# Kernel optimization log

Measured on AMD Instinct MI355X. Metric: run time of the kernel, lower is better.

Reference implementation:

```python
import jax, jax.numpy as jnp
import numpy as np
from jax import lax

S, D_IN, D_FC, H_LSTM, H_RNN, D_OUT = 16384, 6, 20, 48, 24, 2


def _lstm_layer(seq, Wih, Whh, bih, bhh):
    # seq: [S, d_in]; PyTorch gate order: i, f, g, o
    H = Whh.shape[1]
    xW = seq @ Wih.T + (bih + bhh)  # [S, 4H] precomputed input projections

    def step(carry, xw):
        h, c = carry
        g = xw + h @ Whh.T
        i = jax.nn.sigmoid(g[:H])
        f = jax.nn.sigmoid(g[H:2 * H])
        gg = jnp.tanh(g[2 * H:3 * H])
        o = jax.nn.sigmoid(g[3 * H:])
        c = f * c + i * gg
        h = o * jnp.tanh(c)
        return (h, c), h

    z = jnp.zeros((H,), seq.dtype)
    _, hs = lax.scan(step, (z, z), xW)
    return hs  # [S, H]


def _rnn_layer(seq, Wih, Whh, bih, bhh):
    H = Whh.shape[1]
    xW = seq @ Wih.T + (bih + bhh)

    def step(h, xw):
        h = jnp.tanh(xw + h @ Whh.T)
        return h, h

    _, hs = lax.scan(step, jnp.zeros((H,), seq.dtype), xW)
    return hs


def setup_inputs() -> dict:
    key = jax.random.key(0)
    ks = iter(jax.random.split(key, 32))

    def p(shape, fan_in):
        s = 1.0 / np.sqrt(fan_in)
        return jax.random.uniform(next(ks), shape, jnp.float32, -s, s)

    inp = {"x": jax.random.normal(next(ks), (S, D_IN), jnp.float32)}
    inp["fc1_W"] = p((D_FC, D_IN), D_IN)
    inp["fc1_b"] = p((D_FC,), D_IN)
    inp["fc2_W"] = p((D_FC, D_FC), D_FC)
    inp["fc2_b"] = p((D_FC,), D_FC)
    # LSTM layer 0: input 20 -> hidden 48
    inp["lstm0_Wih"] = p((4 * H_LSTM, D_FC), H_LSTM)
    inp["lstm0_Whh"] = p((4 * H_LSTM, H_LSTM), H_LSTM)
    inp["lstm0_bih"] = p((4 * H_LSTM,), H_LSTM)
    inp["lstm0_bhh"] = p((4 * H_LSTM,), H_LSTM)
    # LSTM layers 1..4: input 48 -> hidden 48, stacked
    inp["lstmr_Wih"] = p((4, 4 * H_LSTM, H_LSTM), H_LSTM)
    inp["lstmr_Whh"] = p((4, 4 * H_LSTM, H_LSTM), H_LSTM)
    inp["lstmr_bih"] = p((4, 4 * H_LSTM), H_LSTM)
    inp["lstmr_bhh"] = p((4, 4 * H_LSTM), H_LSTM)
    # RNN layer 0: 48 -> 24, layer 1: 24 -> 24
    inp["rnn0_Wih"] = p((H_RNN, H_LSTM), H_RNN)
    inp["rnn0_Whh"] = p((H_RNN, H_RNN), H_RNN)
    inp["rnn0_bih"] = p((H_RNN,), H_RNN)
    inp["rnn0_bhh"] = p((H_RNN,), H_RNN)
    inp["rnn1_Wih"] = p((H_RNN, H_RNN), H_RNN)
    inp["rnn1_Whh"] = p((H_RNN, H_RNN), H_RNN)
    inp["rnn1_bih"] = p((H_RNN,), H_RNN)
    inp["rnn1_bhh"] = p((H_RNN,), H_RNN)
    inp["fc4_W"] = p((D_OUT, H_RNN), H_RNN)
    inp["fc4_b"] = p((D_OUT,), H_RNN)
    return inp


def reference(x, fc1_W, fc1_b, fc2_W, fc2_b,
              lstm0_Wih, lstm0_Whh, lstm0_bih, lstm0_bhh,
              lstmr_Wih, lstmr_Whh, lstmr_bih, lstmr_bhh,
              rnn0_Wih, rnn0_Whh, rnn0_bih, rnn0_bhh,
              rnn1_Wih, rnn1_Whh, rnn1_bih, rnn1_bhh,
              fc4_W, fc4_b):
    h = jax.nn.relu(x @ fc1_W.T + fc1_b)
    h = jax.nn.relu(h @ fc2_W.T + fc2_b)
    h = _lstm_layer(h, lstm0_Wih, lstm0_Whh, lstm0_bih, lstm0_bhh)
    for l in range(4):  # fixed small layer loop
        h = _lstm_layer(h, lstmr_Wih[l], lstmr_Whh[l], lstmr_bih[l], lstmr_bhh[l])
    h = _rnn_layer(h, rnn0_Wih, rnn0_Whh, rnn0_bih, rnn0_bhh)
    h = _rnn_layer(h, rnn1_Wih, rnn1_Whh, rnn1_bih, rnn1_bhh)
    h = jax.nn.relu(h)
    out = h @ fc4_W.T + fc4_b  # [S, 2]
    return out[None]  # [1, S, 2] matching batch_first torch output
```

## Files before the change

### kernel.cpp

```cpp
#include <hip/hip_runtime.h>
#include <hip/hip_bf16.h>

#define S_LEN 16384
#define N_IN 23
#define CH2 32
#define NCH2 (S_LEN / CH2)
#define RING_D 8

#define XW_PAR_F4 1632
#define XW_FLOATS (2 * XW_PAR_F4 * 4)
#define L2E   1.442695041f
#define TWO_L2E 2.885390082f

typedef float v2f __attribute__((ext_vector_type(2)));
typedef _Float16 h2v __attribute__((ext_vector_type(2)));

__device__ __forceinline__ float fexp2(float x) {
#if __has_builtin(__builtin_amdgcn_exp2f)
    return __builtin_amdgcn_exp2f(x);
#else
    return exp2f(x);
#endif
}
__device__ __forceinline__ float fsig(float x) {
    return __builtin_amdgcn_rcpf(1.f + __expf(-x));
}
__device__ __forceinline__ float ftanh_fast(float x) {
    float e = __expf(-2.f * fabsf(x));
    float r = (1.f - e) * __builtin_amdgcn_rcpf(1.f + e);
    return x >= 0.f ? r : -r;
}
__device__ __forceinline__ float rlane(float v, int k) {
    return __uint_as_float(__builtin_amdgcn_readlane(__float_as_uint(v), k));
}
__device__ __forceinline__ h2v rlane_h2(h2v v, int k) {
    int b;
    __builtin_memcpy(&b, &v, 4);
    b = __builtin_amdgcn_readlane(b, k);
    h2v r;
    __builtin_memcpy(&r, &b, 4);
    return r;
}
__device__ __forceinline__ h2v pack_h2(float a, float b) {
    auto p = __builtin_amdgcn_cvt_pkrtz(a, b);
    h2v r;
    __builtin_memcpy(&r, &p, 4);
    return r;
}
__device__ __forceinline__ float dpp_xor1(float v) {
    int b = __float_as_int(v);
    int r = __builtin_amdgcn_update_dpp(b, b, 0xB1, 0xF, 0xF, false);
    return __int_as_float(r);
}

#if __has_builtin(__builtin_amdgcn_fdot2)
__device__ __forceinline__ float fdot2_hw(h2v w, h2v h, float acc) {
    return __builtin_amdgcn_fdot2(w, h, acc, false);
}
#define FDOT2(w, h, acc) fdot2_hw((w), (h), (acc))
#else
__device__ __forceinline__ float fdot2_sw(h2v w, h2v h, float acc) {
    return acc + (float)w.x * (float)h.x + (float)w.y * (float)h.y;
}
#define FDOT2(w, h, acc) fdot2_sw((w), (h), (acc))
#endif

__global__ void detect_kernel(const void* probe, int nsamp, int* flag)
{
    if (blockIdx.x == 0 && threadIdx.x == 0) {
        const unsigned short* p = (const unsigned short*)probe;
        int isbf16 = 1;
        for (int i = 0; i < nsamp; i++) {
            float v = __uint_as_float(((unsigned int)p[i]) << 16);
            if (!(fabsf(v) < 1e4f)) { isbf16 = 0; break; }
        }
        *flag = isbf16;
    }
}

struct IngestArgs {
    const void* src[N_IN];
    float*      dst[N_IN];
    int         n[N_IN];
};

__global__ void ingest_kernel(IngestArgs args, const int* __restrict__ flag)
{
    const int isbf16 = *flag;
    const int tid    = blockIdx.x * blockDim.x + threadIdx.x;
    const int stride = gridDim.x * blockDim.x;
    for (int i = 0; i < N_IN; i++) {
        const int n = args.n[i];
        float* dst  = args.dst[i];
        if (isbf16) {
            const unsigned short* s = (const unsigned short*)args.src[i];
            for (int j = tid; j < n; j += stride)
                dst[j] = __uint_as_float(((unsigned int)s[j]) << 16);
        } else {
            const float* s = (const float*)args.src[i];
            for (int j = tid; j < n; j += stride)
                dst[j] = s[j];
        }
    }
}

__global__ void init_kernel(int* prog)
{
    int t = threadIdx.x;
    if (t < 1024) prog[t] = 0;
}

__global__ void fc12_kernel(const float* __restrict__ x,
                            const float* __restrict__ W1, const float* __restrict__ b1,
                            const float* __restrict__ W2, const float* __restrict__ b2,
                            float* __restrict__ h2out)
{
    int s = blockIdx.x * blockDim.x + threadIdx.x;
    if (s >= S_LEN) return;
    float xin[6];
#pragma unroll
    for (int k = 0; k < 6; k++) xin[k] = x[s * 6 + k];
    float h1[20];
#pragma unroll
    for (int j = 0; j < 20; j++) {
        float a = b1[j];
#pragma unroll
        for (int k = 0; k < 6; k++) a += W1[j * 6 + k] * xin[k];
        h1[j] = a > 0.f ? a : 0.f;
    }
#pragma unroll
    for (int j = 0; j < 20; j++) {
        float a = b2[j];
#pragma unroll
        for (int k = 0; k < 20; k++) a += W2[j * 20 + k] * h1[k];
        h2out[s * 20 + j] = a > 0.f ? a : 0.f;
    }
}

template <int DIN, int NG, bool TRANS>
__device__ void producer_block(const float* __restrict__ in,
                               const float* __restrict__ Wih,
                               const float* __restrict__ bih,
                               const float* __restrict__ bhh,
                               float* __restrict__ ring,
                               int* my_prog, int* in_prog, int* cons_prog,
                               float* smem)
{
    constexpr int GR  = NG / 3;
    constexpr int GS  = 256 / GR;
    constexpr int SLT = CH2 / GS;

    const int t  = threadIdx.x;
    const int rg = t % GR;
    const int sg = t / GR;

    float* in_sh = smem;
    float* xw_sh = smem + CH2 * DIN;

    float w[3][DIN];
    float bs[3];
    int cellr[3], partr[3];
#pragma unroll
    for (int r = 0; r < 3; r++) {
        const int row = rg * 3 + r;
        const float fac = TRANS ? ((row / 48) == 2 ? TWO_L2E : L2E) : 1.f;
#pragma unroll
        for (int k = 0; k < DIN; k++) w[r][k] = Wih[row * DIN + k] * fac;
        bs[r] = (bih[row] + bhh[row]) * fac;
        cellr[r] = row % 48;
        partr[r] = row / 48;
    }

    const float4* x4 = (const float4*)in_sh;

    for (int c = 0; c < NCH2; c++) {
        if (t == 0) {
            if (in_prog) {
                while (__hip_atomic_load(in_prog, __ATOMIC_ACQUIRE, __HIP_MEMORY_SCOPE_AGENT) < c + 1)
                    __builtin_amdgcn_s_sleep(1);
            }
            if (c >= RING_D) {
                while (__hip_atomic_load(cons_prog, __ATOMIC_ACQUIRE, __HIP_MEMORY_SCOPE_AGENT) < c - RING_D + 1)
                    __builtin_amdgcn_s_sleep(1);
            }
        }
        __syncthreads();
        {
            const float4* gsrc = (const float4*)(in + (size_t)c * CH2 * DIN);
            float4* ldst = (float4*)in_sh;
            for (int i = t; i < CH2 * DIN / 4; i += 256) ldst[i] = gsrc[i];
        }
        __syncthreads();

#pragma unroll
        for (int i = 0; i < SLT; i++) {
            const int sl = sg * SLT + i;
            float a0 = bs[0], a1 = bs[1], a2 = bs[2];
#pragma unroll
            for (int k = 0; k < DIN / 4; k++) {
                float4 xv = x4[sl * (DIN / 4) + k];
                a0 += w[0][4 * k + 0] * xv.x; a0 += w[0][4 * k + 1] * xv.y;
                a0 += w[0][4 * k + 2] * xv.z; a0 += w[0][4 * k + 3] * xv.w;
                a1 += w[1][4 * k + 0] * xv.x; a1 += w[1][4 * k + 1] * xv.y;
                a1 += w[1][4 * k + 2] * xv.z; a1 += w[1][4 * k + 3] * xv.w;
                a2 += w[2][4 * k + 0] * xv.x; a2 += w[2][4 * k + 1] * xv.y;
                a2 += w[2][4 * k + 2] * xv.z; a2 += w[2][4 * k + 3] * xv.w;
            }
            if (TRANS) {
                xw_sh[(sl * 48 + cellr[0]) * 4 + partr[0]] = a0;
                xw_sh[(sl * 48 + cellr[1]) * 4 + partr[1]] = a1;
                xw_sh[(sl * 48 + cellr[2]) * 4 + partr[2]] = a2;
            } else {
                xw_sh[sl * NG + rg * 3 + 0] = a0;
                xw_sh[sl * NG + rg * 3 + 1] = a1;
                xw_sh[sl * NG + rg * 3 + 2] = a2;
            }
        }
        __syncthreads();
        {
            const float4* lsrc = (const float4*)xw_sh;
            float4* gdst = (float4*)(ring + (size_t)(c % RING_D) * CH2 * NG);
            for (int i = t; i < CH2 * NG / 4; i += 256) gdst[i] = lsrc[i];
        }
        __syncthreads();
        if (t == 0)
            __hip_atomic_store(my_prog, c + 1, __ATOMIC_RELEASE, __HIP_MEMORY_SCOPE_AGENT);
    }
}

__device__ void lstm_scan(const float* __restrict__ Whh,
                          const float* __restrict__ ring,
                          float* __restrict__ hseq,
                          int* my_prog, int* prod_prog, float* smem)
{
    const int t = threadIdx.x;
    const int j = (t < 48) ? t : 47;
    float* xw_buf = smem;
    float* hh_buf = smem + XW_FLOATS;

    h2v wI[24], wF[24], wG[24], wO[24];
    if (t < 64) {
#pragma unroll
        for (int k = 0; k < 24; k++) {
            wI[k] = pack_h2(Whh[j * 48 + 2 * k] * L2E,           Whh[j * 48 + 2 * k + 1] * L2E);
            wF[k] = pack_h2(Whh[(48 + j) * 48 + 2 * k] * L2E,    Whh[(48 + j) * 48 + 2 * k + 1] * L2E);
            wG[k] = pack_h2(Whh[(96 + j) * 48 + 2 * k] * TWO_L2E, Whh[(96 + j) * 48 + 2 * k + 1] * TWO_L2E);
            wO[k] = pack_h2(Whh[(144 + j) * 48 + 2 * k] * L2E,   Whh[(144 + j) * 48 + 2 * k + 1] * L2E);
        }
    }
    const int jo = j + (j >> 4);
    float hvec = 0.f, ccell = 0.f;

    if (t >= 128) {
        while (__hip_atomic_load(prod_prog, __ATOMIC_ACQUIRE, __HIP_MEMORY_SCOPE_AGENT) < 1)
            __builtin_amdgcn_s_sleep(8);
        const float4* g = (const float4*)ring;
        float4* d = (float4*)xw_buf;
        for (int i = t - 128; i < CH2 * 48; i += 128) d[i + (i >> 4)] = g[i];
    }
    __syncthreads();

    for (int c = 0; c < NCH2; c++) {
        if (t < 64) {
            const float4* xf = (const float4*)xw_buf + (c & 1) * XW_PAR_F4;
            float* hh = hh_buf + (c & 1) * (CH2 * 48);
            float4 xw4 = xf[jo];
            for (int sl = 0; sl < CH2; sl++) {
                float4 nxt = xf[(sl + 1) * 51 + jo];
                float hn = dpp_xor1(hvec);
                h2v hp = pack_h2(hvec, hn);
                float aI0 = xw4.x, aF0 = xw4.y, aG0 = xw4.z, aO0 = xw4.w;
                float aI1 = 0.f, aF1 = 0.f, aG1 = 0.f, aO1 = 0.f;
#pragma unroll
                for (int kp = 0; kp < 12; kp++) {
                    h2v hb = rlane_h2(hp, 2 * kp);
                    aI0 = FDOT2(wI[kp], hb, aI0);
                    aF0 = FDOT2(wF[kp], hb, aF0);
                    aG0 = FDOT2(wG[kp], hb, aG0);
                    aO0 = FDOT2(wO[kp], hb, aO0);
                }
#pragma unroll
                for (int kp = 12; kp < 24; kp++) {
                    h2v hb = rlane_h2(hp, 2 * kp);
                    aI1 = FDOT2(wI[kp], hb, aI1);
                    aF1 = FDOT2(wF[kp], hb, aF1);
                    aG1 = FDOT2(wG[kp], hb, aG1);
                    aO1 = FDOT2(wO[kp], hb, aO1);
                }
                float aI = aI0 + aI1, aF = aF0 + aF1;
                float aG = aG0 + aG1, aO = aO0 + aO1;
                float eI = fexp2(-aI);
                float eF = fexp2(-aF);
                float eG = fexp2(-fabsf(aG));
                float eO = fexp2(-aO);
                float fv = __builtin_amdgcn_rcpf(1.f + eF);
                float ig = (1.f - eG) * __builtin_amdgcn_rcpf((1.f + eI) * (1.f + eG));
                ig = __int_as_float(__float_as_int(ig) ^
                                    (__float_as_int(aG) & 0x80000000));
                ccell = fmaf(fv, ccell, ig);
                float eC = fexp2(-TWO_L2E * fabsf(ccell));
                float r  = (1.f - eC) * __builtin_amdgcn_rcpf((1.f + eO) * (1.f + eC));
                float h  = __int_as_float(__float_as_int(r) ^
                                          (__float_as_int(ccell) & 0x80000000));
                hvec = h;
                if (t < 48) hh[sl * 48 + t] = h;
                xw4 = nxt;
            }
        } else if (t < 128) {
            if (c >= 1) {
                const float4* s4 = (const float4*)(hh_buf + ((c - 1) & 1) * (CH2 * 48));
                float4* d4 = (float4*)(hseq + (size_t)(c - 1) * CH2 * 48);
                for (int i = t - 64; i < CH2 * 12; i += 64) d4[i] = s4[i];
                if (t == 64)
                    __hip_atomic_store(my_prog, c, __ATOMIC_RELEASE, __HIP_MEMORY_SCOPE_AGENT);
            }
        } else {
            if (c + 1 < NCH2) {
                while (__hip_atomic_load(prod_prog, __ATOMIC_ACQUIRE, __HIP_MEMORY_SCOPE_AGENT) < c + 2)
                    __builtin_amdgcn_s_sleep(8);
                const float4* g = (const float4*)(ring + (size_t)((c + 1) % RING_D) * CH2 * 192);
                float4* d = (float4*)xw_buf + ((c + 1) & 1) * XW_PAR_F4;
                for (int i = t - 128; i < CH2 * 48; i += 128) d[i + (i >> 4)] = g[i];
            }
        }
        __syncthreads();
    }
    if (t >= 64 && t < 128) {
        const float4* s4 = (const float4*)(hh_buf + ((NCH2 - 1) & 1) * (CH2 * 48));
        float4* d4 = (float4*)(hseq + (size_t)(NCH2 - 1) * CH2 * 48);
        for (int i = t - 64; i < CH2 * 12; i += 64) d4[i] = s4[i];
        if (t == 64)
            __hip_atomic_store(my_prog, NCH2, __ATOMIC_RELEASE, __HIP_MEMORY_SCOPE_AGENT);
    }
}

__device__ void rnn_scan(const float* __restrict__ Whh,
                         const float* __restrict__ ring,
                         float* __restrict__ hseq,
                         int* my_prog, int* prod_prog, float* smem)
{
    const int t = threadIdx.x;
    float* xw_buf = smem;
    float* hh_buf = smem + 1536;

    float whh[24];
    if (t < 24) {
#pragma unroll
        for (int k = 0; k < 24; k++) whh[k] = Whh[t * 24 + k];
    }
    float hvec = 0.f;

    if (t >= 128) {
        while (__hip_atomic_load(prod_prog, __ATOMIC_ACQUIRE, __HIP_MEMORY_SCOPE_AGENT) < 1)
            __builtin_amdgcn_s_sleep(8);
        const float4* g = (const float4*)ring;
        float4* d = (float4*)xw_buf;
        for (int i = t - 128; i < CH2 * 6; i += 128) d[i] = g[i];
    }
    __syncthreads();

    for (int c = 0; c < NCH2; c++) {
        if (t < 64) {
            const float* xwc = xw_buf + (c & 1) * (CH2 * 24);
            float* hh = hh_buf + (c & 1) * (CH2 * 24);
            float xwv = (t < 24) ? xwc[t] : 0.f;
            for (int sl = 0; sl < CH2; sl++) {
                float nxtx = (t < 24) ? xwc[((sl + 1 < CH2) ? sl + 1 : sl) * 24 + t] : 0.f;
                float a0 = xwv, a1 = 0.f, a2 = 0.f, a3 = 0.f;
#pragma unroll
                for (int k = 0; k < 24; k += 4) {
                    a0 += rlane(hvec, k + 0) * whh[k + 0];
                    a1 += rlane(hvec, k + 1) * whh[k + 1];
                    a2 += rlane(hvec, k + 2) * whh[k + 2];
                    a3 += rlane(hvec, k + 3) * whh[k + 3];
                }
                float h = ftanh_fast((a0 + a1) + (a2 + a3));
                if (t < 24) {
                    hvec = h;
                    hh[sl * 24 + t] = h;
                }
                xwv = nxtx;
            }
        } else if (t < 128) {
            if (c >= 1) {
                const float4* s4 = (const float4*)(hh_buf + ((c - 1) & 1) * (CH2 * 24));
                float4* d4 = (float4*)(hseq + (size_t)(c - 1) * CH2 * 24);
                for (int i = t - 64; i < CH2 * 6; i += 64) d4[i] = s4[i];
                if (t == 64)
                    __hip_atomic_store(my_prog, c, __ATOMIC_RELEASE, __HIP_MEMORY_SCOPE_AGENT);
            }
        } else {
            if (c + 1 < NCH2) {
                while (__hip_atomic_load(prod_prog, __ATOMIC_ACQUIRE, __HIP_MEMORY_SCOPE_AGENT) < c + 2)
                    __builtin_amdgcn_s_sleep(8);
                const float4* g = (const float4*)(ring + (size_t)((c + 1) % RING_D) * CH2 * 24);
                float4* d = (float4*)(xw_buf + ((c + 1) & 1) * (CH2 * 24));
                for (int i = t - 128; i < CH2 * 6; i += 128) d[i] = g[i];
            }
        }
        __syncthreads();
    }
    if (t >= 64 && t < 128) {
        const float4* s4 = (const float4*)(hh_buf + ((NCH2 - 1) & 1) * (CH2 * 24));
        float4* d4 = (float4*)(hseq + (size_t)(NCH2 - 1) * CH2 * 24);
        for (int i = t - 64; i < CH2 * 6; i += 64) d4[i] = s4[i];
        if (t == 64)
            __hip_atomic_store(my_prog, NCH2, __ATOMIC_RELEASE, __HIP_MEMORY_SCOPE_AGENT);
    }
}

struct PipeArgs {
    const float* h2;
    const float* l0_Wih; const float* l0_Whh; const float* l0_bih; const float* l0_bhh;
    const float* lr_Wih; const float* lr_Whh; const float* lr_bih; const float* lr_bhh;
    const float* r0_Wih; const float* r0_Whh; const float* r0_bih; const float* r0_bhh;
    const float* r1_Wih; const float* r1_Whh; const float* r1_bih; const float* r1_bhh;
    float* seq0; float* seq1; float* seq2; float* seq3; float* seq4;
    float* rnnA; float* rnnB;
    float* ring[7];
    int* prog;
};

__global__ void __launch_bounds__(256, 1) pipeline_kernel(PipeArgs a)
{
    __shared__ __align__(16) float smem[16128];
    const int b = blockIdx.x;
    const float* seqin[7] = {a.h2, a.seq0, a.seq1, a.seq2, a.seq3, a.seq4, a.rnnA};
    float* seqout[7] = {a.seq0, a.seq1, a.seq2, a.seq3, a.seq4, a.rnnA, a.rnnB};
    int* sp[7]; int* pp[7];
    for (int l = 0; l < 7; l++) { sp[l] = a.prog + l * 64; pp[l] = a.prog + (8 + l) * 64; }

    if (b < 7) {
        const int l = b;
        int* inp = (l == 0) ? nullptr : sp[l - 1];
        if (l == 0) {
            producer_block<20, 192, true>(a.h2, a.l0_Wih, a.l0_bih, a.l0_bhh,
                                          a.ring[0], pp[0], inp, sp[0], smem);
        } else if (l <= 4) {
            producer_block<48, 192, true>(seqin[l],
                                          a.lr_Wih + (size_t)(l - 1) * 192 * 48,
                                          a.lr_bih + (size_t)(l - 1) * 192,
                                          a.lr_bhh + (size_t)(l - 1) * 192,
                                          a.ring[l], pp[l], inp, sp[l], smem);
        } else if (l == 5) {
            producer_block<48, 24, false>(a.seq4, a.r0_Wih, a.r0_bih, a.r0_bhh,
                                          a.ring[5], pp[5], inp, sp[5], smem);
        } else {
            producer_block<24, 24, false>(a.rnnA, a.r1_Wih, a.r1_bih, a.r1_bhh,
                                          a.ring[6], pp[6], inp, sp[6], smem);
        }
    } else {
        const int l = b - 7;
        if (l == 0) {
            lstm_scan(a.l0_Whh, a.ring[0], seqout[0], sp[0], pp[0], smem);
        } else if (l <= 4) {
            lstm_scan(a.lr_Whh + (size_t)(l - 1) * 192 * 48,
                      a.ring[l], seqout[l], sp[l], pp[l], smem);
        } else if (l == 5) {
            rnn_scan(a.r0_Whh, a.ring[5], seqout[5], sp[5], pp[5], smem);
        } else {
            rnn_scan(a.r1_Whh, a.ring[6], seqout[6], sp[6], pp[6], smem);
        }
    }
}

__global__ void out_kernel(const float* __restrict__ hin,
                           const float* __restrict__ W,
                           const float* __restrict__ b,
                           void* __restrict__ out,
                           const int* __restrict__ flag)
{
    int s = blockIdx.x * blockDim.x + threadIdx.x;
    if (s >= S_LEN) return;
    const int isbf16 = *flag;
    float h[24];
#pragma unroll
    for (int k = 0; k < 24; k++) {
        float v = hin[s * 24 + k];
        h[k] = v > 0.f ? v : 0.f;
    }
#pragma unroll
    for (int j = 0; j < 2; j++) {
        float a = b[j];
#pragma unroll
        for (int k = 0; k < 24; k++) a += W[j * 24 + k] * h[k];
        if (isbf16) ((__hip_bfloat16*)out)[s * 2 + j] = __float2bfloat16(a);
        else        ((float*)out)[s * 2 + j] = a;
    }
}

extern "C" void kernel_launch(void* const* d_in, const int* in_sizes, int n_in,
                              void* d_out, int out_size, void* d_ws, size_t ws_size,
                              hipStream_t stream)
{
    int*   ip    = (int*)d_ws;
    int*   flag  = ip;
    int*   prog  = ip + 256;
    float* ws    = (float*)d_ws;
    float* conv0 = ws + 4096;

    IngestArgs ia;
    float* conv[N_IN];
    {
        float* p = conv0;
        for (int i = 0; i < N_IN; i++) {
            conv[i] = p;
            ia.src[i] = d_in[i];
            ia.dst[i] = p;
            ia.n[i]   = in_sizes[i];
            p += in_sizes[i];
        }
    }
    float* h2   = conv0 + 191000;
    float* seq0 = h2 + 327680;
    float* seq1 = seq0 + 786432;
    float* seq2 = seq1 + 786432;
    float* seq3 = seq2 + 786432;
    float* seq4 = seq3 + 786432;
    float* rnnA = seq4 + 786432;
    float* rnnB = rnnA + 393216;
    float* rbase = rnnB + 393216;
    float* ring[7];
    {
        float* p = rbase;
        for (int l = 0; l < 5; l++) { ring[l] = p; p += RING_D * CH2 * 192; }
        for (int l = 5; l < 7; l++) { ring[l] = p; p += RING_D * CH2 * 24;  }
    }

    const int TPB = 256;
    const int NB  = S_LEN / TPB;

    detect_kernel<<<1, 64, 0, stream>>>(d_in[1], in_sizes[1], flag);
    ingest_kernel<<<128, 256, 0, stream>>>(ia, flag);
    init_kernel<<<1, 1024, 0, stream>>>(prog);

    fc12_kernel<<<NB, TPB, 0, stream>>>(conv[0], conv[1], conv[2], conv[3], conv[4], h2);

    PipeArgs pa;
    pa.h2 = h2;
    pa.l0_Wih = conv[5];  pa.l0_Whh = conv[6];  pa.l0_bih = conv[7];  pa.l0_bhh = conv[8];
    pa.lr_Wih = conv[9];  pa.lr_Whh = conv[10]; pa.lr_bih = conv[11]; pa.lr_bhh = conv[12];
    pa.r0_Wih = conv[13]; pa.r0_Whh = conv[14]; pa.r0_bih = conv[15]; pa.r0_bhh = conv[16];
    pa.r1_Wih = conv[17]; pa.r1_Whh = conv[18]; pa.r1_bih = conv[19]; pa.r1_bhh = conv[20];
    pa.seq0 = seq0; pa.seq1 = seq1; pa.seq2 = seq2; pa.seq3 = seq3; pa.seq4 = seq4;
    pa.rnnA = rnnA; pa.rnnB = rnnB;
    for (int l = 0; l < 7; l++) pa.ring[l] = ring[l];
    pa.prog = prog;

    pipeline_kernel<<<14, 256, 0, stream>>>(pa);

    out_kernel<<<NB, TPB, 0, stream>>>(rnnB, conv[21], conv[22], d_out, flag);
}
```

Measured before the change: 5.536 ms.

## Interleave two recurrent layers per wavefront with a chunk lag to hide latency

Each scan block now runs two consecutive recurrent layers (LSTM+LSTM or LSTM+RNN), offset by a fixed chunk lag. Their independent step chains are interleaved in one wavefront so the dependency latency of one layer's recurrence can be filled with the other's work. Chunk size is halved to shorten the pipeline fill, the padded shared-memory layout is dropped, and the launch goes from 14 to 11 blocks. The cost is double the weight registers per thread and more synchronisation points per chunk, and the halved chunk alters the ring buffer depth, which may cost throughput.

Result: slower. 9.692 ms (+75.1%).

```diff
diff --git a/kernel.cpp b/kernel.cpp
--- a/kernel.cpp
+++ b/kernel.cpp
@@ -3,16 +3,14 @@
 
 #define S_LEN 16384
 #define N_IN 23
-#define CH2 32
+#define CH2 16
 #define NCH2 (S_LEN / CH2)
 #define RING_D 8
-
-#define XW_PAR_F4 1632
-#define XW_FLOATS (2 * XW_PAR_F4 * 4)
-#define L2E   1.442695041f
+#define LAG 6
+
+#define L2E     1.442695041f
 #define TWO_L2E 2.885390082f
 
-typedef float v2f __attribute__((ext_vector_type(2)));
 typedef _Float16 h2v __attribute__((ext_vector_type(2)));
 
 __device__ __forceinline__ float fexp2(float x) {
@@ -21,9 +19,6 @@
 #else
     return exp2f(x);
 #endif
-}
-__device__ __forceinline__ float fsig(float x) {
-    return __builtin_amdgcn_rcpf(1.f + __expf(-x));
 }
 __device__ __forceinline__ float ftanh_fast(float x) {
     float e = __expf(-2.f * fabsf(x));
@@ -148,7 +143,7 @@
 {
     constexpr int GR  = NG / 3;
     constexpr int GS  = 256 / GR;
-    constexpr int SLT = CH2 / GS;
+    constexpr int SLT = (CH2 + GS - 1) / GS;
 
     const int t  = threadIdx.x;
     const int rg = t % GR;
@@ -195,25 +190,27 @@
 #pragma unroll
         for (int i = 0; i < SLT; i++) {
             const int sl = sg * SLT + i;
-            float a0 = bs[0], a1 = bs[1], a2 = bs[2];
-#pragma unroll
-            for (int k = 0; k < DIN / 4; k++) {
-                float4 xv = x4[sl * (DIN / 4) + k];
-                a0 += w[0][4 * k + 0] * xv.x; a0 += w[0][4 * k + 1] * xv.y;
-                a0 += w[0][4 * k + 2] * xv.z; a0 += w[0][4 * k + 3] * xv.w;
-                a1 += w[1][4 * k + 0] * xv.x; a1 += w[1][4 * k + 1] * xv.y;
-                a1 += w[1][4 * k + 2] * xv.z; a1 += w[1][4 * k + 3] * xv.w;
-                a2 += w[2][4 * k + 0] * xv.x; a2 += w[2][4 * k + 1] * xv.y;
-                a2 += w[2][4 * k + 2] * xv.z; a2 += w[2][4 * k + 3] * xv.w;
-            }
-            if (TRANS) {
-                xw_sh[(sl * 48 + cellr[0]) * 4 + partr[0]] = a0;
-                xw_sh[(sl * 48 + cellr[1]) * 4 + partr[1]] = a1;
-                xw_sh[(sl * 48 + cellr[2]) * 4 + partr[2]] = a2;
-            } else {
-                xw_sh[sl * NG + rg * 3 + 0] = a0;
-                xw_sh[sl * NG + rg * 3 + 1] = a1;
-                xw_sh[sl * NG + rg * 3 + 2] = a2;
+            if (sl < CH2) {
+                float a0 = bs[0], a1 = bs[1], a2 = bs[2];
+#pragma unroll
+                for (int k = 0; k < DIN / 4; k++) {
+                    float4 xv = x4[sl * (DIN / 4) + k];
+                    a0 += w[0][4 * k + 0] * xv.x; a0 += w[0][4 * k + 1] * xv.y;
+                    a0 += w[0][4 * k + 2] * xv.z; a0 += w[0][4 * k + 3] * xv.w;
+                    a1 += w[1][4 * k + 0] * xv.x; a1 += w[1][4 * k + 1] * xv.y;
+                    a1 += w[1][4 * k + 2] * xv.z; a1 += w[1][4 * k + 3] * xv.w;
+                    a2 += w[2][4 * k + 0] * xv.x; a2 += w[2][4 * k + 1] * xv.y;
+                    a2 += w[2][4 * k + 2] * xv.z; a2 += w[2][4 * k + 3] * xv.w;
+                }
+                if (TRANS) {
+                    xw_sh[(sl * 48 + cellr[0]) * 4 + partr[0]] = a0;
+                    xw_sh[(sl * 48 + cellr[1]) * 4 + partr[1]] = a1;
+                    xw_sh[(sl * 48 + cellr[2]) * 4 + partr[2]] = a2;
+                } else {
+                    xw_sh[sl * NG + rg * 3 + 0] = a0;
+                    xw_sh[sl * NG + rg * 3 + 1] = a1;
+                    xw_sh[sl * NG + rg * 3 + 2] = a2;
+                }
             }
         }
         __syncthreads();
@@ -228,109 +225,271 @@
     }
 }
 
-__device__ void lstm_scan(const float* __restrict__ Whh,
-                          const float* __restrict__ ring,
-                          float* __restrict__ hseq,
-                          int* my_prog, int* prod_prog, float* smem)
+__device__ __forceinline__ void lstm_step(
+    const h2v (&wI)[24], const h2v (&wF)[24], const h2v (&wG)[24], const h2v (&wO)[24],
+    const float4* __restrict__ xfl,
+    int sl, float4& xw4, float& hvec, float& ccell,
+    float*& hst, int hstr)
+{
+    float4 nxt = xfl[(sl + 1) * 48];
+    float hn = dpp_xor1(hvec);
+    h2v hp = pack_h2(hvec, hn);
+    float aI = xw4.x, aF = xw4.y, aG = xw4.z, aO = xw4.w;
+#pragma unroll
+    for (int kp = 0; kp < 24; kp++) {
+        h2v hb = rlane_h2(hp, 2 * kp);
+        aI = FDOT2(wI[kp], hb, aI);
+        aF = FDOT2(wF[kp], hb, aF);
+        aG = FDOT2(wG[kp], hb, aG);
+        aO = FDOT2(wO[kp], hb, aO);
+    }
+    float eI = fexp2(-aI);
+    float eF = fexp2(-aF);
+    float eG = fexp2(-fabsf(aG));
+    float eO = fexp2(-aO);
+    float fv = __builtin_amdgcn_rcpf(1.f + eF);
+    float ig = (1.f - eG) * __builtin_amdgcn_rcpf((1.f + eI) * (1.f + eG));
+    ig = __int_as_float(__float_as_int(ig) ^ (__float_as_int(aG) & 0x80000000));
+    ccell = fmaf(fv, ccell, ig);
+    float eC = fexp2(-TWO_L2E * fabsf(ccell));
+    float r  = (1.f - eC) * __builtin_amdgcn_rcpf((1.f + eO) * (1.f + eC));
+    float h  = __int_as_float(__float_as_int(r) ^ (__float_as_int(ccell) & 0x80000000));
+    hvec = h;
+    *hst = h; hst += hstr;
+    xw4 = nxt;
+}
+
+__device__ __forceinline__ void lstm_load_w(const float* __restrict__ Whh, int j,
+    h2v (&wI)[24], h2v (&wF)[24], h2v (&wG)[24], h2v (&wO)[24])
+{
+#pragma unroll
+    for (int k = 0; k < 24; k++) {
+        wI[k] = pack_h2(Whh[j * 48 + 2 * k] * L2E,            Whh[j * 48 + 2 * k + 1] * L2E);
+        wF[k] = pack_h2(Whh[(48 + j) * 48 + 2 * k] * L2E,     Whh[(48 + j) * 48 + 2 * k + 1] * L2E);
+        wG[k] = pack_h2(Whh[(96 + j) * 48 + 2 * k] * TWO_L2E, Whh[(96 + j) * 48 + 2 * k + 1] * TWO_L2E);
+        wO[k] = pack_h2(Whh[(144 + j) * 48 + 2 * k] * L2E,    Whh[(144 + j) * 48 + 2 * k + 1] * L2E);
+    }
+}
+
+__device__ __forceinline__ void rnn_step(
+    const float (&whh)[24], const float* __restrict__ xwc,
+    int sl, float& xwv, float& hvec, float*& hst, int hstr, int tB)
+{
+    float nxtx = xwc[(sl + 1) * 24 + tB];
+    float a0 = xwv, a1 = 0.f, a2 = 0.f, a3 = 0.f;
+#pragma unroll
+    for (int k = 0; k < 24; k += 4) {
+        a0 += rlane(hvec, k + 0) * whh[k + 0];
+        a1 += rlane(hvec, k + 1) * whh[k + 1];
+        a2 += rlane(hvec, k + 2) * whh[k + 2];
+        a3 += rlane(hvec, k + 3) * whh[k + 3];
+    }
+    float h = ftanh_fast((a0 + a1) + (a2 + a3));
+    hvec = h;
+    *hst = h; hst += hstr;
+    xwv = nxtx;
+}
+
+__device__ void lstm_scan_pair(
+    const float* __restrict__ WhhA, const float* __restrict__ ringA,
+    float* __restrict__ hseqA, int* spA, int* ppA,
+    const float* __restrict__ WhhB, const float* __restrict__ ringB,
+    float* __restrict__ hseqB, int* spB, int* ppB,
+    float* __restrict__ smem)
 {
     const int t = threadIdx.x;
     const int j = (t < 48) ? t : 47;
-    float* xw_buf = smem;
-    float* hh_buf = smem + XW_FLOATS;
-
-    h2v wI[24], wF[24], wG[24], wO[24];
+    float* xwA  = smem;
+    float* xwB  = smem + 6144;
+    float* hhA  = smem + 12288;
+    float* hhB  = smem + 13824;
+    float* dump = smem + 15360;
+
+    h2v wIA[24], wFA[24], wGA[24], wOA[24];
+    h2v wIB[24], wFB[24], wGB[24], wOB[24];
     if (t < 64) {
-#pragma unroll
-        for (int k = 0; k < 24; k++) {
-            wI[k] = pack_h2(Whh[j * 48 + 2 * k] * L2E,           Whh[j * 48 + 2 * k + 1] * L2E);
-            wF[k] = pack_h2(Whh[(48 + j) * 48 + 2 * k] * L2E,    Whh[(48 + j) * 48 + 2 * k + 1] * L2E);
-            wG[k] = pack_h2(Whh[(96 + j) * 48 + 2 * k] * TWO_L2E, Whh[(96 + j) * 48 + 2 * k + 1] * TWO_L2E);
-            wO[k] = pack_h2(Whh[(144 + j) * 48 + 2 * k] * L2E,   Whh[(144 + j) * 48 + 2 * k + 1] * L2E);
-        }
-    }
-    const int jo = j + (j >> 4);
-    float hvec = 0.f, ccell = 0.f;
+        lstm_load_w(WhhA, j, wIA, wFA, wGA, wOA);
+        lstm_load_w(WhhB, j, wIB, wFB, wGB, wOB);
+    }
+    float hA = 0.f, cAc = 0.f, hB = 0.f, cBc = 0.f;
+    const int hstr = (t < 48) ? 48 : 0;
 
     if (t >= 128) {
-        while (__hip_atomic_load(prod_prog, __ATOMIC_ACQUIRE, __HIP_MEMORY_SCOPE_AGENT) < 1)
+        while (__hip_atomic_load(ppA, __ATOMIC_ACQUIRE, __HIP_MEMORY_SCOPE_AGENT) < 1)
             __builtin_amdgcn_s_sleep(8);
-        const float4* g = (const float4*)ring;
-        float4* d = (float4*)xw_buf;
-        for (int i = t - 128; i < CH2 * 48; i += 128) d[i + (i >> 4)] = g[i];
+        const float4* g = (const float4*)ringA;
+        float4* d = (float4*)xwA;
+        for (int i = t - 128; i < CH2 * 48; i += 128) d[i] = g[i];
     }
     __syncthreads();
 
-    for (int c = 0; c < NCH2; c++) {
+    for (int cc = 0; cc < NCH2 + LAG; cc++) {
+        const int ca = cc, cb = cc - LAG;
+        const bool Aact = ca < NCH2;
+        const bool Bact = cb >= 0;
         if (t < 64) {
-            const float4* xf = (const float4*)xw_buf + (c & 1) * XW_PAR_F4;
-            float* hh = hh_buf + (c & 1) * (CH2 * 48);
-            float4 xw4 = xf[jo];
-            for (int sl = 0; sl < CH2; sl++) {
-                float4 nxt = xf[(sl + 1) * 51 + jo];
-                float hn = dpp_xor1(hvec);
-                h2v hp = pack_h2(hvec, hn);
-                float aI0 = xw4.x, aF0 = xw4.y, aG0 = xw4.z, aO0 = xw4.w;
-                float aI1 = 0.f, aF1 = 0.f, aG1 = 0.f, aO1 = 0.f;
-#pragma unroll
-                for (int kp = 0; kp < 12; kp++) {
-                    h2v hb = rlane_h2(hp, 2 * kp);
-                    aI0 = FDOT2(wI[kp], hb, aI0);
-                    aF0 = FDOT2(wF[kp], hb, aF0);
-                    aG0 = FDOT2(wG[kp], hb, aG0);
-                    aO0 = FDOT2(wO[kp], hb, aO0);
+            const float4* xfA = (const float4*)(xwA + (ca & 1) * (CH2 * 192)) + j;
+            const float4* xfB = (const float4*)(xwB + (cb & 1) * (CH2 * 192)) + j;
+            float* hsA = (t < 48) ? (hhA + (ca & 1) * (CH2 * 48) + t) : (dump + (t - 48));
+            float* hsB = (t < 48) ? (hhB + (cb & 1) * (CH2 * 48) + t) : (dump + (t - 48));
+            float4 xwa, xwb;
+            if (Aact) xwa = xfA[0];
+            if (Bact) xwb = xfB[0];
+            if (Aact && Bact) {
+                for (int sl = 0; sl < CH2; sl++) {
+                    lstm_step(wIA, wFA, wGA, wOA, xfA, sl, xwa, hA, cAc, hsA, hstr);
+                    lstm_step(wIB, wFB, wGB, wOB, xfB, sl, xwb, hB, cBc, hsB, hstr);
                 }
-#pragma unroll
-                for (int kp = 12; kp < 24; kp++) {
-                    h2v hb = rlane_h2(hp, 2 * kp);
-                    aI1 = FDOT2(wI[kp], hb, aI1);
-                    aF1 = FDOT2(wF[kp], hb, aF1);
-                    aG1 = FDOT2(wG[kp], hb, aG1);
-                    aO1 = FDOT2(wO[kp], hb, aO1);
-                }
-                float aI = aI0 + aI1, aF = aF0 + aF1;
-                float aG = aG0 + aG1, aO = aO0 + aO1;
-                float eI = fexp2(-aI);
-                float eF = fexp2(-aF);
-                float eG = fexp2(-fabsf(aG));
-                float eO = fexp2(-aO);
-                float fv = __builtin_amdgcn_rcpf(1.f + eF);
-                float ig = (1.f - eG) * __builtin_amdgcn_rcpf((1.f + eI) * (1.f + eG));
-                ig = __int_as_float(__float_as_int(ig) ^
-                                    (__float_as_int(aG) & 0x80000000));
-                ccell = fmaf(fv, ccell, ig);
-                float eC = fexp2(-TWO_L2E * fabsf(ccell));
-                float r  = (1.f - eC) * __builtin_amdgcn_rcpf((1.f + eO) * (1.f + eC));
-                float h  = __int_as_float(__float_as_int(r) ^
-                                          (__float_as_int(ccell) & 0x80000000));
-                hvec = h;
-                if (t < 48) hh[sl * 48 + t] = h;
-                xw4 = nxt;
+            } else if (Aact) {
+                for (int sl = 0; sl < CH2; sl++)
+                    lstm_step(wIA, wFA, wGA, wOA, xfA, sl, xwa, hA, cAc, hsA, hstr);
+            } else if (Bact) {
+                for (int sl = 0; sl < CH2; sl++)
+                    lstm_step(wIB, wFB, wGB, wOB, xfB, sl, xwb, hB, cBc, hsB, hstr);
             }
         } else if (t < 128) {
-            if (c >= 1) {
-                const float4* s4 = (const float4*)(hh_buf + ((c - 1) & 1) * (CH2 * 48));
-                float4* d4 = (float4*)(hseq + (size_t)(c - 1) * CH2 * 48);
+            if (ca >= 1 && ca <= NCH2) {
+                const float4* s4 = (const float4*)(hhA + ((ca - 1) & 1) * (CH2 * 48));
+                float4* d4 = (float4*)(hseqA + (size_t)(ca - 1) * CH2 * 48);
                 for (int i = t - 64; i < CH2 * 12; i += 64) d4[i] = s4[i];
-                if (t == 64)
-                    __hip_atomic_store(my_prog, c, __ATOMIC_RELEASE, __HIP_MEMORY_SCOPE_AGENT);
+            }
+            if (cb >= 1) {
+                const float4* s4 = (const float4*)(hhB + ((cb - 1) & 1) * (CH2 * 48));
+                float4* d4 = (float4*)(hseqB + (size_t)(cb - 1) * CH2 * 48);
+                for (int i = t - 64; i < CH2 * 12; i += 64) d4[i] = s4[i];
+            }
+            if (t == 64) {
+                if (ca >= 1 && ca <= NCH2)
+                    __hip_atomic_store(spA, ca, __ATOMIC_RELEASE, __HIP_MEMORY_SCOPE_AGENT);
+                if (cb >= 1)
+                    __hip_atomic_store(spB, cb, __ATOMIC_RELEASE, __HIP_MEMORY_SCOPE_AGENT);
             }
         } else {
-            if (c + 1 < NCH2) {
-                while (__hip_atomic_load(prod_prog, __ATOMIC_ACQUIRE, __HIP_MEMORY_SCOPE_AGENT) < c + 2)
+            if (ca + 1 < NCH2) {
+                while (__hip_atomic_load(ppA, __ATOMIC_ACQUIRE, __HIP_MEMORY_SCOPE_AGENT) < ca + 2)
                     __builtin_amdgcn_s_sleep(8);
-                const float4* g = (const float4*)(ring + (size_t)((c + 1) % RING_D) * CH2 * 192);
-                float4* d = (float4*)xw_buf + ((c + 1) & 1) * XW_PAR_F4;
-                for (int i = t - 128; i < CH2 * 48; i += 128) d[i + (i >> 4)] = g[i];
+                const float4* g = (const float4*)(ringA + (size_t)((ca + 1) % RING_D) * CH2 * 192);
+                float4* d = (float4*)(xwA + ((ca + 1) & 1) * (CH2 * 192));
+                for (int i = t - 128; i < CH2 * 48; i += 128) d[i] = g[i];
+            }
+            if (cb + 1 >= 0 && cb + 1 < NCH2) {
+                while (__hip_atomic_load(ppB, __ATOMIC_ACQUIRE, __HIP_MEMORY_SCOPE_AGENT) < cb + 2)
+                    __builtin_amdgcn_s_sleep(8);
+                const float4* g = (const float4*)(ringB + (size_t)((cb + 1) % RING_D) * CH2 * 192);
+                float4* d = (float4*)(xwB + ((cb + 1) & 1) * (CH2 * 192));
+                for (int i = t - 128; i < CH2 * 48; i += 128) d[i] = g[i];
             }
         }
         __syncthreads();
     }
     if (t >= 64 && t < 128) {
-        const float4* s4 = (const float4*)(hh_buf + ((NCH2 - 1) & 1) * (CH2 * 48));
-        float4* d4 = (float4*)(hseq + (size_t)(NCH2 - 1) * CH2 * 48);
+        const float4* s4 = (const float4*)(hhB + ((NCH2 - 1) & 1) * (CH2 * 48));
+        float4* d4 = (float4*)(hseqB + (size_t)(NCH2 - 1) * CH2 * 48);
         for (int i = t - 64; i < CH2 * 12; i += 64) d4[i] = s4[i];
         if (t == 64)
-            __hip_atomic_store(my_prog, NCH2, __ATOMIC_RELEASE, __HIP_MEMORY_SCOPE_AGENT);
+            __hip_atomic_store(spB, NCH2, __ATOMIC_RELEASE, __HIP_MEMORY_SCOPE_AGENT);
+    }
+}
+
+__device__ void lstm_rnn_pair(
+    const float* __restrict__ WhhA, const float* __restrict__ ringA,
+    float* __restrict__ hseqA, int* spA, int* ppA,
+    const float* __restrict__ WhhB, const float* __restrict__ ringB,
+    float* __restrict__ hseqB, int* spB, int* ppB,
+    float* __restrict__ smem)
+{
+    const int t = threadIdx.x;
+    const int j  = (t < 48) ? t : 47;
+    const int tB = (t < 24) ? t : 23;
+    float* xwA  = smem;
+    float* hhA  = smem + 6144;
+    float* xwB  = smem + 7680;
+    float* hhB  = smem + 8448;
+    float* dump = smem + 9216;
+
+    h2v wIA[24], wFA[24], wGA[24], wOA[24];
+    float whhB[24];
+    if (t < 64) lstm_load_w(WhhA, j, wIA, wFA, wGA, wOA);
+#pragma unroll
+    for (int k = 0; k < 24; k++) whhB[k] = WhhB[tB * 24 + k];
+    float hA = 0.f, cAc = 0.f, hB = 0.f;
+    const int hstrA = (t < 48) ? 48 : 0;
+    const int hstrB = (t < 24) ? 24 : 0;
+
+    if (t >= 128) {
+        while (__hip_atomic_load(ppA, __ATOMIC_ACQUIRE, __HIP_MEMORY_SCOPE_AGENT) < 1)
+            __builtin_amdgcn_s_sleep(8);
+        const float4* g = (const float4*)ringA;
+        float4* d = (float4*)xwA;
+        for (int i = t - 128; i < CH2 * 48; i += 128) d[i] = g[i];
+    }
+    __syncthreads();
+
+    for (int cc = 0; cc < NCH2 + LAG; cc++) {
+        const int ca = cc, cb = cc - LAG;
+        const bool Aact = ca < NCH2;
+        const bool Bact = cb >= 0;
+        if (t < 64) {
+            const float4* xfA = (const float4*)(xwA + (ca & 1) * (CH2 * 192)) + j;
+            const float* xwcB = xwB + (cb & 1) * (CH2 * 24);
+            float* hsA = (t < 48) ? (hhA + (ca & 1) * (CH2 * 48) + t) : (dump + (t - 48));
+            float* hsB = (t < 24) ? (hhB + (cb & 1) * (CH2 * 24) + t) : (dump + (t - 24));
+            float4 xwa; float xwb = 0.f;
+            if (Aact) xwa = xfA[0];
+            if (Bact) xwb = xwcB[tB];
+            if (Aact && Bact) {
+                for (int sl = 0; sl < CH2; sl++) {
+                    lstm_step(wIA, wFA, wGA, wOA, xfA, sl, xwa, hA, cAc, hsA, hstrA);
+                    rnn_step(whhB, xwcB, sl, xwb, hB, hsB, hstrB, tB);
+                }
+            } else if (Aact) {
+                for (int sl = 0; sl < CH2; sl++)
+                    lstm_step(wIA, wFA, wGA, wOA, xfA, sl, xwa, hA, cAc, hsA, hstrA);
+            } else if (Bact) {
+                for (int sl = 0; sl < CH2; sl++)
+                    rnn_step(whhB, xwcB, sl, xwb, hB, hsB, hstrB, tB);
+            }
+        } else if (t < 128) {
+            if (ca >= 1 && ca <= NCH2) {
+                const float4* s4 = (const float4*)(hhA + ((ca - 1) & 1) * (CH2 * 48));
+                float4* d4 = (float4*)(hseqA + (size_t)(ca - 1) * CH2 * 48);
+                for (int i = t - 64; i < CH2 * 12; i += 64) d4[i] = s4[i];
+            }
+            if (cb >= 1) {
+                const float4* s4 = (const float4*)(hhB + ((cb - 1) & 1) * (CH2 * 24));
+                float4* d4 = (float4*)(hseqB + (size_t)(cb - 1) * CH2 * 24);
+                for (int i = t - 64; i < CH2 * 6; i += 64) d4[i] = s4[i];
+            }
+            if (t == 64) {
+                if (ca >= 1 && ca <= NCH2)
+                    __hip_atomic_store(spA, ca, __ATOMIC_RELEASE, __HIP_MEMORY_SCOPE_AGENT);
+                if (cb >= 1)
+                    __hip_atomic_store(spB, cb, __ATOMIC_RELEASE, __HIP_MEMORY_SCOPE_AGENT);
+            }
+        } else {
+            if (ca + 1 < NCH2) {
+                while (__hip_atomic_load(ppA, __ATOMIC_ACQUIRE, __HIP_MEMORY_SCOPE_AGENT) < ca + 2)
+                    __builtin_amdgcn_s_sleep(8);
+                const float4* g = (const float4*)(ringA + (size_t)((ca + 1) % RING_D) * CH2 * 192);
+                float4* d = (float4*)(xwA + ((ca + 1) & 1) * (CH2 * 192));
+                for (int i = t - 128; i < CH2 * 48; i += 128) d[i] = g[i];
+            }
+            if (cb + 1 >= 0 && cb + 1 < NCH2) {
+                while (__hip_atomic_load(ppB, __ATOMIC_ACQUIRE, __HIP_MEMORY_SCOPE_AGENT) < cb + 2)
+                    __builtin_amdgcn_s_sleep(8);
+                const float4* g = (const float4*)(ringB + (size_t)((cb + 1) % RING_D) * CH2 * 24);
+                float4* d = (float4*)(xwB + ((cb + 1) & 1) * (CH2 * 24));
+                for (int i = t - 128; i < CH2 * 6; i += 128) d[i] = g[i];
+            }
+        }
+        __syncthreads();
+    }
+    if (t >= 64 && t < 128) {
+        const float4* s4 = (const float4*)(hhB + ((NCH2 - 1) & 1) * (CH2 * 24));
+        float4* d4 = (float4*)(hseqB + (size_t)(NCH2 - 1) * CH2 * 24);
+        for (int i = t - 64; i < CH2 * 6; i += 64) d4[i] = s4[i];
+        if (t == 64)
+            __hip_atomic_store(spB, NCH2, __ATOMIC_RELEASE, __HIP_MEMORY_SCOPE_AGENT);
     }
 }
 
@@ -423,10 +582,9 @@
 
 __global__ void __launch_bounds__(256, 1) pipeline_kernel(PipeArgs a)
 {
-    __shared__ __align__(16) float smem[16128];
+    __shared__ __align__(16) float smem[15424];
     const int b = blockIdx.x;
     const float* seqin[7] = {a.h2, a.seq0, a.seq1, a.seq2, a.seq3, a.seq4, a.rnnA};
-    float* seqout[7] = {a.seq0, a.seq1, a.seq2, a.seq3, a.seq4, a.rnnA, a.rnnB};
     int* sp[7]; int* pp[7];
     for (int l = 0; l < 7; l++) { sp[l] = a.prog + l * 64; pp[l] = a.prog + (8 + l) * 64; }
 
@@ -449,18 +607,17 @@
             producer_block<24, 24, false>(a.rnnA, a.r1_Wih, a.r1_bih, a.r1_bhh,
                                           a.ring[6], pp[6], inp, sp[6], smem);
         }
+    } else if (b == 7) {
+        lstm_scan_pair(a.l0_Whh, a.ring[0], a.seq0, sp[0], pp[0],
+                       a.lr_Whh,  a.ring[1], a.seq1, sp[1], pp[1], smem);
+    } else if (b == 8) {
+        lstm_scan_pair(a.lr_Whh + (size_t)1 * 192 * 48, a.ring[2], a.seq2, sp[2], pp[2],
+                       a.lr_Whh + (size_t)2 * 192 * 48, a.ring[3], a.seq3, sp[3], pp[3], smem);
+    } else if (b == 9) {
+        lstm_rnn_pair(a.lr_Whh + (size_t)3 * 192 * 48, a.ring[4], a.seq4, sp[4], pp[4],
+                      a.r0_Whh, a.ring[5], a.rnnA, sp[5], pp[5], smem);
     } else {
-        const int l = b - 7;
-        if (l == 0) {
-            lstm_scan(a.l0_Whh, a.ring[0], seqout[0], sp[0], pp[0], smem);
-        } else if (l <= 4) {
-            lstm_scan(a.lr_Whh + (size_t)(l - 1) * 192 * 48,
-                      a.ring[l], seqout[l], sp[l], pp[l], smem);
-        } else if (l == 5) {
-            rnn_scan(a.r0_Whh, a.ring[5], seqout[5], sp[5], pp[5], smem);
-        } else {
-            rnn_scan(a.r1_Whh, a.ring[6], seqout[6], sp[6], pp[6], smem);
-        }
+        rnn_scan(a.r1_Whh, a.ring[6], a.rnnB, sp[6], pp[6], smem);
     }
 }
 
@@ -547,7 +704,7 @@
     for (int l = 0; l < 7; l++) pa.ring[l] = ring[l];
     pa.prog = prog;
 
-    pipeline_kernel<<<14, 256, 0, stream>>>(pa);
+    pipeline_kernel<<<11, 256, 0, stream>>>(pa);
 
     out_kernel<<<NB, TPB, 0, stream>>>(rnnB, conv[21], conv[22], d_out, flag);
 }
```

## Split LSTM recurrent gates across four waves with per-step LDS exchange

Applied to the files above, without the earlier changes.

The LSTM scan used to run all four gate dot-products in a single wave, holding 96 packed weight registers per lane. Now each of the four waves computes one gate, and the gate pre-activations are exchanged each timestep through a double-buffered LDS slot guarded by a block barrier. The producer writes xW in a gate-major transposed layout so each wave reads its own gate slice. The separate copy-in and copy-out waves are folded into all-thread phases between chunks. This shortens the per-step dot-product chain and lowers register pressure, but adds a __syncthreads and LDS round trip to every one of the 16384 serial steps.

Result: slower. 8.061 ms (+45.6%).

```diff
diff --git a/kernel.cpp b/kernel.cpp
--- a/kernel.cpp
+++ b/kernel.cpp
@@ -7,12 +7,13 @@
 #define NCH2 (S_LEN / CH2)
 #define RING_D 8
 
-#define XW_PAR_F4 1632
-#define XW_FLOATS (2 * XW_PAR_F4 * 4)
-#define L2E   1.442695041f
+#define L2E     1.442695041f
 #define TWO_L2E 2.885390082f
 
-typedef float v2f __attribute__((ext_vector_type(2)));
+#define HH_OFF 12288
+#define EX_OFF 15360
+#define SMEM_F 15872
+
 typedef _Float16 h2v __attribute__((ext_vector_type(2)));
 
 __device__ __forceinline__ float fexp2(float x) {
@@ -21,9 +22,6 @@
 #else
     return exp2f(x);
 #endif
-}
-__device__ __forceinline__ float fsig(float x) {
-    return __builtin_amdgcn_rcpf(1.f + __expf(-x));
 }
 __device__ __forceinline__ float ftanh_fast(float x) {
     float e = __expf(-2.f * fabsf(x));
@@ -207,9 +205,9 @@
                 a2 += w[2][4 * k + 2] * xv.z; a2 += w[2][4 * k + 3] * xv.w;
             }
             if (TRANS) {
-                xw_sh[(sl * 48 + cellr[0]) * 4 + partr[0]] = a0;
-                xw_sh[(sl * 48 + cellr[1]) * 4 + partr[1]] = a1;
-                xw_sh[(sl * 48 + cellr[2]) * 4 + partr[2]] = a2;
+                xw_sh[(partr[0] * CH2 + sl) * 48 + cellr[0]] = a0;
+                xw_sh[(partr[1] * CH2 + sl) * 48 + cellr[1]] = a1;
+                xw_sh[(partr[2] * CH2 + sl) * 48 + cellr[2]] = a2;
             } else {
                 xw_sh[sl * NG + rg * 3 + 0] = a0;
                 xw_sh[sl * NG + rg * 3 + 1] = a1;
@@ -233,104 +231,94 @@
                           float* __restrict__ hseq,
                           int* my_prog, int* prod_prog, float* smem)
 {
-    const int t = threadIdx.x;
-    const int j = (t < 48) ? t : 47;
-    float* xw_buf = smem;
-    float* hh_buf = smem + XW_FLOATS;
-
-    h2v wI[24], wF[24], wG[24], wO[24];
-    if (t < 64) {
-#pragma unroll
-        for (int k = 0; k < 24; k++) {
-            wI[k] = pack_h2(Whh[j * 48 + 2 * k] * L2E,           Whh[j * 48 + 2 * k + 1] * L2E);
-            wF[k] = pack_h2(Whh[(48 + j) * 48 + 2 * k] * L2E,    Whh[(48 + j) * 48 + 2 * k + 1] * L2E);
-            wG[k] = pack_h2(Whh[(96 + j) * 48 + 2 * k] * TWO_L2E, Whh[(96 + j) * 48 + 2 * k + 1] * TWO_L2E);
-            wO[k] = pack_h2(Whh[(144 + j) * 48 + 2 * k] * L2E,   Whh[(144 + j) * 48 + 2 * k + 1] * L2E);
-        }
-    }
-    const int jo = j + (j >> 4);
+    const int t  = threadIdx.x;
+    const int w  = t >> 6;
+    const int ln = t & 63;
+    const int j  = (ln < 48) ? ln : 47;
+    float* xw = smem;
+    float* hh = smem + HH_OFF;
+    float* ex = smem + EX_OFF;
+
+    const float fac = (w == 2) ? TWO_L2E : L2E;
+    h2v wv[24];
+#pragma unroll
+    for (int k = 0; k < 24; k++)
+        wv[k] = pack_h2(Whh[(w * 48 + j) * 48 + 2 * k] * fac,
+                        Whh[(w * 48 + j) * 48 + 2 * k + 1] * fac);
+
+    const int exw = w * 64 + ln;
     float hvec = 0.f, ccell = 0.f;
 
-    if (t >= 128) {
+    if (t == 0) {
         while (__hip_atomic_load(prod_prog, __ATOMIC_ACQUIRE, __HIP_MEMORY_SCOPE_AGENT) < 1)
             __builtin_amdgcn_s_sleep(8);
+    }
+    __syncthreads();
+    {
         const float4* g = (const float4*)ring;
-        float4* d = (float4*)xw_buf;
-        for (int i = t - 128; i < CH2 * 48; i += 128) d[i + (i >> 4)] = g[i];
+        float4* d = (float4*)xw;
+        for (int i = t; i < CH2 * 48; i += 256) d[i] = g[i];
     }
     __syncthreads();
 
+    int p = 0;
     for (int c = 0; c < NCH2; c++) {
-        if (t < 64) {
-            const float4* xf = (const float4*)xw_buf + (c & 1) * XW_PAR_F4;
-            float* hh = hh_buf + (c & 1) * (CH2 * 48);
-            float4 xw4 = xf[jo];
-            for (int sl = 0; sl < CH2; sl++) {
-                float4 nxt = xf[(sl + 1) * 51 + jo];
-                float hn = dpp_xor1(hvec);
-                h2v hp = pack_h2(hvec, hn);
-                float aI0 = xw4.x, aF0 = xw4.y, aG0 = xw4.z, aO0 = xw4.w;
-                float aI1 = 0.f, aF1 = 0.f, aG1 = 0.f, aO1 = 0.f;
-#pragma unroll
-                for (int kp = 0; kp < 12; kp++) {
-                    h2v hb = rlane_h2(hp, 2 * kp);
-                    aI0 = FDOT2(wI[kp], hb, aI0);
-                    aF0 = FDOT2(wF[kp], hb, aF0);
-                    aG0 = FDOT2(wG[kp], hb, aG0);
-                    aO0 = FDOT2(wO[kp], hb, aO0);
-                }
-#pragma unroll
-                for (int kp = 12; kp < 24; kp++) {
-                    h2v hb = rlane_h2(hp, 2 * kp);
-                    aI1 = FDOT2(wI[kp], hb, aI1);
-                    aF1 = FDOT2(wF[kp], hb, aF1);
-                    aG1 = FDOT2(wG[kp], hb, aG1);
-                    aO1 = FDOT2(wO[kp], hb, aO1);
-                }
-                float aI = aI0 + aI1, aF = aF0 + aF1;
-                float aG = aG0 + aG1, aO = aO0 + aO1;
-                float eI = fexp2(-aI);
-                float eF = fexp2(-aF);
-                float eG = fexp2(-fabsf(aG));
-                float eO = fexp2(-aO);
-                float fv = __builtin_amdgcn_rcpf(1.f + eF);
-                float ig = (1.f - eG) * __builtin_amdgcn_rcpf((1.f + eI) * (1.f + eG));
-                ig = __int_as_float(__float_as_int(ig) ^
-                                    (__float_as_int(aG) & 0x80000000));
-                ccell = fmaf(fv, ccell, ig);
-                float eC = fexp2(-TWO_L2E * fabsf(ccell));
-                float r  = (1.f - eC) * __builtin_amdgcn_rcpf((1.f + eO) * (1.f + eC));
-                float h  = __int_as_float(__float_as_int(r) ^
-                                          (__float_as_int(ccell) & 0x80000000));
-                hvec = h;
-                if (t < 48) hh[sl * 48 + t] = h;
-                xw4 = nxt;
-            }
-        } else if (t < 128) {
-            if (c >= 1) {
-                const float4* s4 = (const float4*)(hh_buf + ((c - 1) & 1) * (CH2 * 48));
-                float4* d4 = (float4*)(hseq + (size_t)(c - 1) * CH2 * 48);
-                for (int i = t - 64; i < CH2 * 12; i += 64) d4[i] = s4[i];
-                if (t == 64)
-                    __hip_atomic_store(my_prog, c, __ATOMIC_RELEASE, __HIP_MEMORY_SCOPE_AGENT);
-            }
-        } else {
-            if (c + 1 < NCH2) {
-                while (__hip_atomic_load(prod_prog, __ATOMIC_ACQUIRE, __HIP_MEMORY_SCOPE_AGENT) < c + 2)
-                    __builtin_amdgcn_s_sleep(8);
-                const float4* g = (const float4*)(ring + (size_t)((c + 1) % RING_D) * CH2 * 192);
-                float4* d = (float4*)xw_buf + ((c + 1) & 1) * XW_PAR_F4;
-                for (int i = t - 128; i < CH2 * 48; i += 128) d[i + (i >> 4)] = g[i];
-            }
-        }
-        __syncthreads();
-    }
-    if (t >= 64 && t < 128) {
-        const float4* s4 = (const float4*)(hh_buf + ((NCH2 - 1) & 1) * (CH2 * 48));
-        float4* d4 = (float4*)(hseq + (size_t)(NCH2 - 1) * CH2 * 48);
-        for (int i = t - 64; i < CH2 * 12; i += 64) d4[i] = s4[i];
-        if (t == 64)
-            __hip_atomic_store(my_prog, NCH2, __ATOMIC_RELEASE, __HIP_MEMORY_SCOPE_AGENT);
+        const float* xwc = xw + (c & 1) * (4 * CH2 * 48) + w * (CH2 * 48);
+        float* hhc = hh + (c & 1) * (CH2 * 48);
+        float xa = xwc[j];
+        for (int sl = 0; sl < CH2; sl++) {
+            float nxt = xwc[(sl + 1) * 48 + j];
+            float hn = dpp_xor1(hvec);
+            h2v hp = pack_h2(hvec, hn);
+            float a0 = xa, a1 = 0.f;
+#pragma unroll
+            for (int kp = 0; kp < 12; kp++) {
+                h2v hb = rlane_h2(hp, 2 * kp);
+                a0 = FDOT2(wv[kp], hb, a0);
+            }
+#pragma unroll
+            for (int kp = 12; kp < 24; kp++) {
+                h2v hb = rlane_h2(hp, 2 * kp);
+                a1 = FDOT2(wv[kp], hb, a1);
+            }
+            ex[p * 256 + exw] = a0 + a1;
+            __syncthreads();
+            const float* exr = ex + p * 256;
+            float aI = exr[j], aF = exr[64 + j], aG = exr[128 + j], aO = exr[192 + j];
+            float eI = fexp2(-aI);
+            float eF = fexp2(-aF);
+            float eG = fexp2(-fabsf(aG));
+            float eO = fexp2(-aO);
+            float fv = __builtin_amdgcn_rcpf(1.f + eF);
+            float ig = (1.f - eG) * __builtin_amdgcn_rcpf((1.f + eI) * (1.f + eG));
+            ig = __int_as_float(__float_as_int(ig) ^ (__float_as_int(aG) & 0x80000000));
+            ccell = fmaf(fv, ccell, ig);
+            float eC = fexp2(-TWO_L2E * fabsf(ccell));
+            float r  = (1.f - eC) * __builtin_amdgcn_rcpf((1.f + eO) * (1.f + eC));
+            float h  = __int_as_float(__float_as_int(r) ^ (__float_as_int(ccell) & 0x80000000));
+            hvec = h;
+            if (t < 48) hhc[sl * 48 + t] = h;
+            xa = nxt;
+            p ^= 1;
+        }
+        if (t == 0 && c + 1 < NCH2) {
+            while (__hip_atomic_load(prod_prog, __ATOMIC_ACQUIRE, __HIP_MEMORY_SCOPE_AGENT) < c + 2)
+                __builtin_amdgcn_s_sleep(8);
+        }
+        __syncthreads();
+        if (c + 1 < NCH2) {
+            const float4* g = (const float4*)(ring + (size_t)((c + 1) % RING_D) * (4 * CH2 * 48));
+            float4* d = (float4*)(xw + ((c + 1) & 1) * (4 * CH2 * 48));
+            for (int i = t; i < CH2 * 48; i += 256) d[i] = g[i];
+        }
+        {
+            const float4* s4 = (const float4*)(hh + (c & 1) * (CH2 * 48));
+            float4* d4 = (float4*)(hseq + (size_t)c * CH2 * 48);
+            for (int i = t; i < CH2 * 12; i += 256) d4[i] = s4[i];
+        }
+        __syncthreads();
+        if (t == 0)
+            __hip_atomic_store(my_prog, c + 1, __ATOMIC_RELEASE, __HIP_MEMORY_SCOPE_AGENT);
     }
 }
 
@@ -423,7 +411,7 @@
 
 __global__ void __launch_bounds__(256, 1) pipeline_kernel(PipeArgs a)
 {
-    __shared__ __align__(16) float smem[16128];
+    __shared__ __align__(16) float smem[SMEM_F];
     const int b = blockIdx.x;
     const float* seqin[7] = {a.h2, a.seq0, a.seq1, a.seq2, a.seq3, a.seq4, a.rnnA};
     float* seqout[7] = {a.seq0, a.seq1, a.seq2, a.seq3, a.seq4, a.rnnA, a.rnnB};
```
